# Kernel optimization log

Measured on AMD Instinct MI355X. Metric: run time of the kernel, lower is better.

Reference implementation:

```python
import jax, jax.numpy as jnp
import numpy as np
from jax import lax

B, N, C = 4, 4096, 512
HEADS, SR = 8, 4
HW = 64  # spatial size, HW*HW == N
EPS = 1e-5


def setup_inputs() -> dict:
    key = jax.random.key(0)
    ks = jax.random.split(key, 12)
    s = 0.02
    return {
        "x": jax.random.normal(ks[0], (B, N, C), jnp.float32),
        "wq": jax.random.normal(ks[1], (C, C), jnp.float32) * s,
        "bq": jnp.zeros((C,), jnp.float32),
        "wk": jax.random.normal(ks[2], (C, C), jnp.float32) * s,
        "bk": jnp.zeros((C,), jnp.float32),
        "wv": jax.random.normal(ks[3], (C, C), jnp.float32) * s,
        "bv": jnp.zeros((C,), jnp.float32),
        "w_sr": jax.random.normal(ks[4], (SR, SR, C, C), jnp.float32) * s,  # HWIO
        "b_sr": jnp.zeros((C,), jnp.float32),
        "gamma": jnp.ones((C,), jnp.float32),
        "beta": jnp.zeros((C,), jnp.float32),
        "wp": jax.random.normal(ks[5], (C, C), jnp.float32) * s,
        "bp": jnp.zeros((C,), jnp.float32),
    }


def _layernorm(x, gamma, beta):
    mu = jnp.mean(x, axis=-1, keepdims=True)
    var = jnp.mean(jnp.square(x - mu), axis=-1, keepdims=True)
    return (x - mu) * lax.rsqrt(var + EPS) * gamma + beta


def reference(x, wq, bq, wk, bk, wv, bv, w_sr, b_sr, gamma, beta, wp, bp):
    b, n, c = x.shape
    dh = c // HEADS
    scale = dh ** (-0.5)
    # Q at full resolution: [b, heads, n, dh]
    q = (x @ wq + bq).reshape(b, n, HEADS, dh).transpose(0, 2, 1, 3)
    # spatial reduction of K/V: conv stride=kernel=SR (VALID)
    xr = x.reshape(b, HW, HW, c)
    xr = lax.conv_general_dilated(
        xr, w_sr, window_strides=(SR, SR), padding="VALID",
        dimension_numbers=("NHWC", "HWIO", "NHWC")) + b_sr
    xr = xr.reshape(b, -1, c)  # [b, n_kv, c]
    xr = _layernorm(xr, gamma, beta)
    n_kv = xr.shape[1]
    k = (xr @ wk + bk).reshape(b, n_kv, HEADS, dh).transpose(0, 2, 1, 3)
    v = (xr @ wv + bv).reshape(b, n_kv, HEADS, dh).transpose(0, 2, 1, 3)
    attn = jnp.einsum("bhqd,bhkd->bhqk", q, k) * scale
    attn = jax.nn.softmax(attn, axis=-1)
    out = jnp.einsum("bhqk,bhkd->bhqd", attn, v)
    out = out.transpose(0, 2, 1, 3).reshape(b, n, c)
    return out @ wp + bp
```

## Files before the change

### kernel.cpp

```cpp
#include <hip/hip_runtime.h>
#include <hip/hip_bf16.h>


#define EPSV 1e-5f
#define SCALE_Q 0.18033688011112042f

typedef __attribute__((ext_vector_type(8))) short short8v;
typedef __attribute__((ext_vector_type(4))) short short4v;
typedef __attribute__((ext_vector_type(4))) float float4v;

static __device__ __forceinline__ ushort f2bf_bits(float x) {
  __hip_bfloat16 h = __float2bfloat16(x);
  return *(ushort*)&h;
}

static __device__ __forceinline__ float4v mfma16(short8v a, short8v b, float4v c) {
  return __builtin_amdgcn_mfma_f32_16x16x32_bf16(a, b, c, 0, 0, 0);
}

static __device__ __forceinline__ size_t img_idx(int row, int k, int KC) {
  const int rt = row >> 7, kc = k >> 5, f = (row >> 4) & 7, lid = row & 15;
  const int k32 = k & 31, lg = (k32 >> 2) & 3, j = (k32 & 3) + ((k32 >> 4) & 1) * 4;
  return ((size_t)(rt * KC + kc) * 8 + f) * 512 + (lid + 16 * lg) * 8 + j;
}

static __device__ __forceinline__ void wr_chunk(ushort* lds, int base, int4 v) {
  *(int2*)&lds[base]       = make_int2(v.x, v.y);
  *(int2*)&lds[base + 128] = make_int2(v.z, v.w);
}

__global__ __launch_bounds__(256)
void prep(const float* __restrict__ x, const float* __restrict__ wq,
          const float* __restrict__ wk, const float* __restrict__ wv,
          const float* __restrict__ wp, const float* __restrict__ wsr,
          const float* __restrict__ bk, const float* __restrict__ bv,
          ushort* __restrict__ xbf, ushort* __restrict__ ximg,
          ushort* __restrict__ wqimg, ushort* __restrict__ wkvimg,
          ushort* __restrict__ wpimg, ushort* __restrict__ wsrT,
          float* __restrict__ bkv) {
  __shared__ float t[32][33];
  const int bid = blockIdx.x, tid = threadIdx.x;
  if (bid < 4096) {
    const int i = bid * 256 + tid;
    const float4* s4 = (const float4*)x;
    const float4 a = s4[2 * i], b = s4[2 * i + 1];
    short8v v;
    v[0] = (short)f2bf_bits(a.x); v[1] = (short)f2bf_bits(a.y);
    v[2] = (short)f2bf_bits(a.z); v[3] = (short)f2bf_bits(a.w);
    v[4] = (short)f2bf_bits(b.x); v[5] = (short)f2bf_bits(b.y);
    v[6] = (short)f2bf_bits(b.z); v[7] = (short)f2bf_bits(b.w);
    *(short8v*)&xbf[(size_t)i * 8] = v;
    const int row = i >> 6, c = (i & 63) * 8;
    const int rt = row >> 7, f = (row >> 4) & 7, lid = row & 15;
    const int kc = c >> 5, k32 = c & 31, lg0 = (k32 >> 2) & 3, j0 = ((k32 >> 4) & 1) * 4;
    ushort* basep = ximg + ((size_t)(rt * 16 + kc) * 8 + f) * 512 + j0;
    const int4 vi = *(const int4*)&v;
    *(int2*)&basep[(lid + 16 * lg0) * 8] = make_int2(vi.x, vi.y);
    *(int2*)&basep[(lid + 16 * (lg0 + 1)) * 8] = make_int2(vi.z, vi.w);
  } else if (bid < 8192) {
    const int tI = bid - 4096;
    const int kr0 = (tI & 255) * 32, c0 = (tI >> 8) * 32;
    {
      const int r = tid >> 3, c4 = (tid & 7) * 4;
      const float4 v = *(const float4*)&wsr[(size_t)(kr0 + r) * 512 + c0 + c4];
      t[r][c4 + 0] = v.x; t[r][c4 + 1] = v.y; t[r][c4 + 2] = v.z; t[r][c4 + 3] = v.w;
    }
    __syncthreads();
    {
      const int n = tid >> 3, k4 = (tid & 7) * 4;
      short4v o;
#pragma unroll
      for (int i = 0; i < 4; ++i) o[i] = (short)f2bf_bits(t[k4 + i][n]);
      *(short4v*)&wsrT[(size_t)(c0 + n) * 8192 + kr0 + k4] = o;
    }
  } else if (bid < 9216) {
    const int wsel = (bid - 8192) >> 8;
    const int tI = (bid - 8192) & 255;
    const int kr0 = (tI & 15) * 32, c0 = (tI >> 4) * 32;
    const float* src = wsel == 0 ? wq : wsel == 1 ? wk : wsel == 2 ? wv : wp;
    ushort* dst = wsel == 0 ? wqimg : wsel == 3 ? wpimg : wkvimg;
    const int colbase = (wsel == 2) ? 512 : 0;
    {
      const int r = tid >> 3, c4 = (tid & 7) * 4;
      const float4 v = *(const float4*)&src[(size_t)(kr0 + r) * 512 + c0 + c4];
      t[r][c4 + 0] = v.x; t[r][c4 + 1] = v.y; t[r][c4 + 2] = v.z; t[r][c4 + 3] = v.w;
    }
    __syncthreads();
    {
      const int n = tid >> 3, k4 = (tid & 7) * 4;
      const int col = colbase + c0 + n, k = kr0 + k4;
      short4v o;
#pragma unroll
      for (int i = 0; i < 4; ++i) o[i] = (short)f2bf_bits(t[k4 + i][n]);
      *(short4v*)&dst[img_idx(col, k, 16)] = o;
    }
  } else {
    const int i4 = tid * 4;
    const float4 v = (i4 < 512) ? *(const float4*)&bk[i4] : *(const float4*)&bv[i4 - 512];
    *(float4*)&bkv[i4] = v;
  }
}

static __device__ __forceinline__ int4 ld_patch(const ushort* xbf, int b, int oh, int ow, int kg) {
  const int ij = kg >> 9, ci = kg & 511;
  const int n = (oh * 4 + (ij >> 2)) * 64 + ow * 4 + (ij & 3);
  return *(const int4*)(xbf + ((size_t)b * 4096 + n) * 512 + ci);
}

__global__ __launch_bounds__(256)
void conv_bf(const ushort* __restrict__ xbf, const ushort* __restrict__ wsrT,
             float* __restrict__ part) {
  __shared__ ushort lds[8192];
  const int tid = threadIdx.x;
  const int wave = tid >> 6, lane = tid & 63;
  const int wm = wave >> 1, wn = wave & 1;
  const int bm = blockIdx.x * 128, bn = blockIdx.y * 128, z = blockIdx.z;
  const int lid = lane & 15, lg = lane >> 4;
  const int r0 = tid >> 2, c8 = tid & 3;
  const int g0 = 2 * (c8 & 1), h2 = c8 >> 1;
  const int c0 = c8 * 8;
  const int basew = ((r0 >> 4) * 64 + 16 * g0 + (r0 & 15)) * 8 + h2 * 4;
  const int p0 = bm + r0, p1 = p0 + 64;
  const int b0 = p0 >> 8, oh0 = (p0 & 255) >> 4, ow0 = p0 & 15;
  const int b1 = p1 >> 8, oh1 = (p1 & 255) >> 4, ow1 = p1 & 15;
  const ushort* Br0 = wsrT + (size_t)(bn + r0) * 8192;
  const ushort* Br1 = Br0 + (size_t)64 * 8192;
  float4v acc[4][4];
  const float4v zf = {0.f, 0.f, 0.f, 0.f};
#pragma unroll
  for (int mi = 0; mi < 4; ++mi)
#pragma unroll
    for (int ni = 0; ni < 4; ++ni) acc[mi][ni] = zf;
  int kg = z * 512 + c0;
  int4 pa0 = ld_patch(xbf, b0, oh0, ow0, kg);
  int4 pa1 = ld_patch(xbf, b1, oh1, ow1, kg);
  int4 pb0 = *(const int4*)(Br0 + kg);
  int4 pb1 = *(const int4*)(Br1 + kg);
  for (int kb = 0; kb < 16; ++kb) {
    wr_chunk(lds, basew, pa0);
    wr_chunk(lds, basew + 2048, pa1);
    wr_chunk(lds, basew + 4096, pb0);
    wr_chunk(lds, basew + 6144, pb1);
    __syncthreads();
    if (kb < 15) {
      kg += 32;
      pa0 = ld_patch(xbf, b0, oh0, ow0, kg);
      pa1 = ld_patch(xbf, b1, oh1, ow1, kg);
      pb0 = *(const int4*)(Br0 + kg);
      pb1 = *(const int4*)(Br1 + kg);
    }
    short8v af[4], bfr[4];
#pragma unroll
    for (int mi = 0; mi < 4; ++mi)
      af[mi] = *(const short8v*)&lds[((wm * 4 + mi) * 64 + lane) * 8];
#pragma unroll
    for (int ni = 0; ni < 4; ++ni)
      bfr[ni] = *(const short8v*)&lds[4096 + ((wn * 4 + ni) * 64 + lane) * 8];
#pragma unroll
    for (int mi = 0; mi < 4; ++mi)
#pragma unroll
      for (int ni = 0; ni < 4; ++ni) acc[mi][ni] = mfma16(af[mi], bfr[ni], acc[mi][ni]);
    __syncthreads();
  }
#pragma unroll
  for (int mi = 0; mi < 4; ++mi)
#pragma unroll
    for (int ni = 0; ni < 4; ++ni)
#pragma unroll
      for (int reg = 0; reg < 4; ++reg)
        part[(size_t)(z * 1024 + bm + wm * 64 + mi * 16 + 4 * lg + reg) * 512 +
             bn + wn * 64 + ni * 16 + lid] = acc[mi][ni][reg];
}

__global__ __launch_bounds__(256)
void reduce_ln(const float* __restrict__ part, const float* __restrict__ bsr,
               const float* __restrict__ gamma, const float* __restrict__ beta,
               ushort* __restrict__ xlnimg) {
  const int wave = threadIdx.x >> 6;
  const int lane = threadIdx.x & 63;
  const int row = blockIdx.x * 4 + wave;
  const int c = lane * 8;
  float v[8];
  {
    const float4 a = *(const float4*)&bsr[c];
    const float4 b = *(const float4*)&bsr[c + 4];
    v[0] = a.x; v[1] = a.y; v[2] = a.z; v[3] = a.w;
    v[4] = b.x; v[5] = b.y; v[6] = b.z; v[7] = b.w;
  }
#pragma unroll
  for (int z = 0; z < 16; ++z) {
    const float* pr = &part[((size_t)z * 1024 + row) * 512 + c];
    const float4 a = *(const float4*)pr;
    const float4 b = *(const float4*)(pr + 4);
    v[0] += a.x; v[1] += a.y; v[2] += a.z; v[3] += a.w;
    v[4] += b.x; v[5] += b.y; v[6] += b.z; v[7] += b.w;
  }
  float sum = 0.f;
#pragma unroll
  for (int i = 0; i < 8; ++i) sum += v[i];
#pragma unroll
  for (int off = 32; off >= 1; off >>= 1) sum += __shfl_xor(sum, off);
  const float mu = sum * (1.0f / 512.0f);
  float sq = 0.f;
#pragma unroll
  for (int i = 0; i < 8; ++i) { v[i] -= mu; sq += v[i] * v[i]; }
#pragma unroll
  for (int off = 32; off >= 1; off >>= 1) sq += __shfl_xor(sq, off);
  const float rs = rsqrtf(sq * (1.0f / 512.0f) + EPSV);
  const float4 g1 = *(const float4*)&gamma[c];
  const float4 g2 = *(const float4*)&gamma[c + 4];
  const float4 e1 = *(const float4*)&beta[c];
  const float4 e2 = *(const float4*)&beta[c + 4];
  const float g[8] = {g1.x, g1.y, g1.z, g1.w, g2.x, g2.y, g2.z, g2.w};
  const float e[8] = {e1.x, e1.y, e1.z, e1.w, e2.x, e2.y, e2.z, e2.w};
  short8v ov;
#pragma unroll
  for (int i = 0; i < 8; ++i) ov[i] = (short)f2bf_bits(v[i] * rs * g[i] + e[i]);
  const int rt = row >> 7, f = (row >> 4) & 7, lid = row & 15;
  const int kc = c >> 5, k32 = c & 31, lg0 = (k32 >> 2) & 3, j0 = ((k32 >> 4) & 1) * 4;
  ushort* basep = xlnimg + ((size_t)(rt * 16 + kc) * 8 + f) * 512 + j0;
  const int4 vi = *(const int4*)&ov;
  *(int2*)&basep[(lid + 16 * lg0) * 8] = make_int2(vi.x, vi.y);
  *(int2*)&basep[(lid + 16 * (lg0 + 1)) * 8] = make_int2(vi.z, vi.w);
}

template<int MODE>
__global__ __launch_bounds__(256)
void gemm_img(const ushort* __restrict__ Aimg, const ushort* __restrict__ Bimg,
              const float* __restrict__ bias, void* __restrict__ outp, float scale) {
  constexpr int KC = 16;
  const int tid = threadIdx.x;
  const int wave = tid >> 6, lane = tid & 63;
  const int wm = wave >> 1, wn = wave & 1;
  const int rt = blockIdx.x, ct = blockIdx.y;
  const int lid = lane & 15, lg = lane >> 4;
  const ushort* Ab = Aimg + ((size_t)rt * KC * 8 + wm * 4) * 512 + lane * 8;
  const ushort* Bb = Bimg + ((size_t)ct * KC * 8 + wn * 4) * 512 + lane * 8;
  float4v acc[4][4];
  const float4v zf = {0.f, 0.f, 0.f, 0.f};
#pragma unroll
  for (int mi = 0; mi < 4; ++mi)
#pragma unroll
    for (int ni = 0; ni < 4; ++ni) acc[mi][ni] = zf;
#pragma unroll
  for (int kb = 0; kb < KC; ++kb) {
    short8v af[4], bf[4];
#pragma unroll
    for (int mi = 0; mi < 4; ++mi)
      af[mi] = *(const short8v*)(Ab + (size_t)kb * 4096 + mi * 512);
#pragma unroll
    for (int ni = 0; ni < 4; ++ni)
      bf[ni] = *(const short8v*)(Bb + (size_t)kb * 4096 + ni * 512);
#pragma unroll
    for (int mi = 0; mi < 4; ++mi)
#pragma unroll
      for (int ni = 0; ni < 4; ++ni) acc[mi][ni] = mfma16(af[mi], bf[ni], acc[mi][ni]);
  }
  float bvv[4];
#pragma unroll
  for (int ni = 0; ni < 4; ++ni) bvv[ni] = bias[ct * 128 + wn * 64 + ni * 16 + lid];
#pragma unroll
  for (int mi = 0; mi < 4; ++mi)
#pragma unroll
    for (int ni = 0; ni < 4; ++ni) {
      const int col = ct * 128 + wn * 64 + ni * 16 + lid;
#pragma unroll
      for (int reg = 0; reg < 4; ++reg) {
        const int row = rt * 128 + wm * 64 + mi * 16 + 4 * lg + reg;
        const float v = (acc[mi][ni][reg] + bvv[ni]) * scale;
        if (MODE == 0) {
          ((float*)outp)[(size_t)row * 512 + col] = v;
        } else if (MODE == 2) {
          ushort* img = (ushort*)outp;
          const int bb = row >> 8, kv = row & 255;
          if (col < 512) {
            const int hh = col >> 6, d = col & 63;
            img[(size_t)(bb * 8 + hh) * 16384 +
                ((kv >> 4) * 2 + (d >> 5)) * 512 +
                ((kv & 15) + (((d >> 2) & 3) << 4)) * 8 +
                (d & 3) + (((d >> 4) & 1) << 2)] = f2bf_bits(v);
          } else {
            const int c2 = col - 512;
            const int hh = c2 >> 6, d = c2 & 63;
            (img + 524288)[(size_t)(bb * 8 + hh) * 16384 +
                ((d >> 4) * 8 + (kv >> 5)) * 512 +
                ((d & 15) + (((kv >> 2) & 3) << 4)) * 8 +
                (kv & 3) + (((kv >> 4) & 1) << 2)] = f2bf_bits(v);
          }
        } else {
          ushort* img = (ushort*)outp;
          const int bq_ = row >> 12, n = row & 4095;
          const int qtt = n >> 7, nn = n & 127;
          const int wv_ = nn >> 5, qf = (nn >> 4) & 1, lidq = nn & 15;
          const int h = col >> 6, d = col & 63, tt = d >> 5, d32 = d & 31;
          const int lgq = (d32 >> 2) & 3, jq = (d32 & 3) + ((d32 >> 4) & 1) * 4;
          img[((size_t)(((bq_ * 8 + h) * 32 + qtt) * 4 + wv_) * 4 + qf * 2 + tt) * 512 +
              (lidq + 16 * lgq) * 8 + jq] = f2bf_bits(v);
        }
      }
    }
}

__global__ __launch_bounds__(256)
void attn_img(const ushort* __restrict__ qimg, const ushort* __restrict__ kvimg,
              ushort* __restrict__ oimg) {
  const int bh = blockIdx.x, qt = blockIdx.y;
  const int b = bh >> 3, h = bh & 7;
  const int tid = threadIdx.x;
  const int wave = tid >> 6, lane = tid & 63;
  const int lid = lane & 15, lg = lane >> 4;
  const ushort* kb_ = kvimg + (size_t)bh * 16384;
  const ushort* vb_ = kvimg + 524288 + (size_t)bh * 16384;
  const ushort* qb_ = qimg + ((size_t)((bh * 32 + qt) * 4 + wave) * 4) * 512 + lane * 8;
  short8v qfr[2][2];
#pragma unroll
  for (int qf = 0; qf < 2; ++qf)
#pragma unroll
    for (int t = 0; t < 2; ++t)
      qfr[qf][t] = *(const short8v*)(qb_ + (qf * 2 + t) * 512);
  float4v s[16][2];
  const float4v zf = {0.f, 0.f, 0.f, 0.f};
#pragma unroll
  for (int kvf = 0; kvf < 16; ++kvf) { s[kvf][0] = zf; s[kvf][1] = zf; }
#pragma unroll
  for (int kvf = 0; kvf < 16; ++kvf)
#pragma unroll
    for (int t = 0; t < 2; ++t) {
      const short8v ka = *(const short8v*)(kb_ + ((kvf * 2 + t) * 64 + lane) * 8);
      s[kvf][0] = mfma16(ka, qfr[0][t], s[kvf][0]);
      s[kvf][1] = mfma16(ka, qfr[1][t], s[kvf][1]);
    }
  float inv[2];
#pragma unroll
  for (int qf = 0; qf < 2; ++qf) {
    float m = -1e30f;
#pragma unroll
    for (int kvf = 0; kvf < 16; ++kvf)
#pragma unroll
      for (int e = 0; e < 4; ++e) m = fmaxf(m, s[kvf][qf][e]);
    m = fmaxf(m, __shfl_xor(m, 16));
    m = fmaxf(m, __shfl_xor(m, 32));
    float sum = 0.f;
#pragma unroll
    for (int kvf = 0; kvf < 16; ++kvf)
#pragma unroll
      for (int e = 0; e < 4; ++e) {
        const float p = __builtin_amdgcn_exp2f(s[kvf][qf][e] - m);
        s[kvf][qf][e] = p;
        sum += p;
      }
    sum += __shfl_xor(sum, 16);
    sum += __shfl_xor(sum, 32);
    inv[qf] = 1.0f / sum;
  }
  float4v o[2][4];
#pragma unroll
  for (int qf = 0; qf < 2; ++qf)
#pragma unroll
    for (int nf = 0; nf < 4; ++nf) o[qf][nf] = zf;
#pragma unroll
  for (int t = 0; t < 8; ++t) {
    short8v vb[4];
#pragma unroll
    for (int nf = 0; nf < 4; ++nf)
      vb[nf] = *(const short8v*)(vb_ + ((nf * 8 + t) * 64 + lane) * 8);
#pragma unroll
    for (int qf = 0; qf < 2; ++qf) {
      short8v pa;
#pragma unroll
      for (int j = 0; j < 4; ++j) {
        pa[j]     = (short)f2bf_bits(s[2 * t][qf][j]);
        pa[4 + j] = (short)f2bf_bits(s[2 * t + 1][qf][j]);
      }
#pragma unroll
      for (int nf = 0; nf < 4; ++nf) o[qf][nf] = mfma16(pa, vb[nf], o[qf][nf]);
    }
  }
  const int rt_o = b * 32 + qt;
#pragma unroll
  for (int qf = 0; qf < 2; ++qf) {
    float sc[4];
#pragma unroll
    for (int reg = 0; reg < 4; ++reg) sc[reg] = __shfl(inv[qf], 4 * lg + reg);
    const int f_o = wave * 2 + qf;
#pragma unroll
    for (int nf = 0; nf < 4; ++nf) {
      const int colc = h * 64 + nf * 16 + lid;
      const int kc = colc >> 5, k32 = colc & 31;
      const int lgk = (k32 >> 2) & 3, jk = (k32 & 3) + ((k32 >> 4) & 1) * 4;
      ushort* basep = oimg + ((size_t)(rt_o * 16 + kc) * 8 + f_o) * 512 + 16 * lgk * 8 + jk;
#pragma unroll
      for (int reg = 0; reg < 4; ++reg)
        basep[(4 * lg + reg) * 8] = f2bf_bits(o[qf][nf][reg] * sc[reg]);
    }
  }
}

extern "C" void kernel_launch(void* const* d_in, const int* in_sizes, int n_in,
                              void* d_out, int out_size, void* d_ws, size_t ws_size,
                              hipStream_t stream) {
  const float* x     = (const float*)d_in[0];
  const float* wq    = (const float*)d_in[1];
  const float* bq    = (const float*)d_in[2];
  const float* wk    = (const float*)d_in[3];
  const float* bk    = (const float*)d_in[4];
  const float* wv    = (const float*)d_in[5];
  const float* bv    = (const float*)d_in[6];
  const float* wsr   = (const float*)d_in[7];
  const float* bsr   = (const float*)d_in[8];
  const float* gamma = (const float*)d_in[9];
  const float* beta  = (const float*)d_in[10];
  const float* wp    = (const float*)d_in[11];
  const float* bp    = (const float*)d_in[12];
  float* out = (float*)d_out;

  char* w = (char*)d_ws;
  ushort* xbf    = (ushort*)(w);
  ushort* ximg   = (ushort*)(w + 16777216);
  float*  part   = (float*) (w + 33554432);
  ushort* qimg   = (ushort*)(w + 33554432);
  ushort* oimg   = (ushort*)(w + 50331648);
  ushort* wsrT   = (ushort*)(w + 67108864);
  ushort* wqimg  = (ushort*)(w + 75497472);
  ushort* wpimg  = (ushort*)(w + 76021760);
  ushort* wkvimg = (ushort*)(w + 76546048);
  ushort* xlnimg = (ushort*)(w + 77594624);
  ushort* kvimg  = (ushort*)(w + 78643200);
  float*  bkv    = (float*) (w + 80740352);

  prep<<<9217, 256, 0, stream>>>(x, wq, wk, wv, wp, wsr, bk, bv,
                                 xbf, ximg, wqimg, wkvimg, wpimg, wsrT, bkv);
  conv_bf<<<dim3(8, 4, 16), 256, 0, stream>>>(xbf, wsrT, part);
  reduce_ln<<<256, 256, 0, stream>>>(part, bsr, gamma, beta, xlnimg);
  gemm_img<2><<<dim3(8, 8), 256, 0, stream>>>(xlnimg, wkvimg, bkv, kvimg, 1.0f);
  gemm_img<3><<<dim3(128, 4), 256, 0, stream>>>(ximg, wqimg, bq, qimg, SCALE_Q);
  attn_img<<<dim3(32, 32), 256, 0, stream>>>(qimg, kvimg, oimg);
  gemm_img<0><<<dim3(128, 4), 256, 0, stream>>>(oimg, wpimg, bp, out, 1.0f);
}
```

Baseline: 231.8 us.

## Fuse conv and Q projection into one launch; stage GEMM tiles via global_load_lds

The spatial-reduction conv and the Q projection GEMM now run as one kernel launch of 1024 blocks. The first 512 blocks do the conv partials and the rest compute Q, so two independent GEMMs can fill the GPU together. The conv weight is pre-laid out in the MFMA image format so it can be loaded with direct global-to-LDS loads. The other GEMMs now stage A/B tiles through LDS with global_load_lds instead of reading fragments straight from global memory. Workspace offsets move so that qimg no longer aliases the conv partial buffer. This adds barrier overhead per k-step in exchange for shared reuse and fewer launches.

```diff
diff --git a/kernel.cpp b/kernel.cpp
--- a/kernel.cpp
+++ b/kernel.cpp
@@ -27,6 +27,12 @@
 static __device__ __forceinline__ void wr_chunk(ushort* lds, int base, int4 v) {
   *(int2*)&lds[base]       = make_int2(v.x, v.y);
   *(int2*)&lds[base + 128] = make_int2(v.z, v.w);
+}
+
+static __device__ __forceinline__ void gl_lds16(const ushort* g, ushort* l) {
+  __builtin_amdgcn_global_load_lds(
+      (const __attribute__((address_space(1))) void*)g,
+      (__attribute__((address_space(3))) void*)l, 16, 0, 0);
 }
 
 __global__ __launch_bounds__(256)
@@ -36,7 +42,7 @@
           const float* __restrict__ bk, const float* __restrict__ bv,
           ushort* __restrict__ xbf, ushort* __restrict__ ximg,
           ushort* __restrict__ wqimg, ushort* __restrict__ wkvimg,
-          ushort* __restrict__ wpimg, ushort* __restrict__ wsrT,
+          ushort* __restrict__ wpimg, ushort* __restrict__ wsrimg,
           float* __restrict__ bkv) {
   __shared__ float t[32][33];
   const int bid = blockIdx.x, tid = threadIdx.x;
@@ -71,7 +77,7 @@
       short4v o;
 #pragma unroll
       for (int i = 0; i < 4; ++i) o[i] = (short)f2bf_bits(t[k4 + i][n]);
-      *(short4v*)&wsrT[(size_t)(c0 + n) * 8192 + kr0 + k4] = o;
+      *(short4v*)&wsrimg[img_idx(c0 + n, kr0 + k4, 256)] = o;
     }
   } else if (bid < 9216) {
     const int wsel = (bid - 8192) >> 8;
@@ -88,11 +94,10 @@
     __syncthreads();
     {
       const int n = tid >> 3, k4 = (tid & 7) * 4;
-      const int col = colbase + c0 + n, k = kr0 + k4;
       short4v o;
 #pragma unroll
       for (int i = 0; i < 4; ++i) o[i] = (short)f2bf_bits(t[k4 + i][n]);
-      *(short4v*)&dst[img_idx(col, k, 16)] = o;
+      *(short4v*)&dst[img_idx(colbase + c0 + n, kr0 + k4, 16)] = o;
     }
   } else {
     const int i4 = tid * 4;
@@ -108,68 +113,112 @@
 }
 
 __global__ __launch_bounds__(256)
-void conv_bf(const ushort* __restrict__ xbf, const ushort* __restrict__ wsrT,
-             float* __restrict__ part) {
+void convq(const ushort* __restrict__ xbf, const ushort* __restrict__ wsrimg,
+           float* __restrict__ part, const ushort* __restrict__ ximg,
+           const ushort* __restrict__ wqimg, const float* __restrict__ bq,
+           ushort* __restrict__ qimg) {
   __shared__ ushort lds[8192];
-  const int tid = threadIdx.x;
+  const int bid = blockIdx.x, tid = threadIdx.x;
   const int wave = tid >> 6, lane = tid & 63;
   const int wm = wave >> 1, wn = wave & 1;
-  const int bm = blockIdx.x * 128, bn = blockIdx.y * 128, z = blockIdx.z;
   const int lid = lane & 15, lg = lane >> 4;
-  const int r0 = tid >> 2, c8 = tid & 3;
-  const int g0 = 2 * (c8 & 1), h2 = c8 >> 1;
-  const int c0 = c8 * 8;
-  const int basew = ((r0 >> 4) * 64 + 16 * g0 + (r0 & 15)) * 8 + h2 * 4;
-  const int p0 = bm + r0, p1 = p0 + 64;
-  const int b0 = p0 >> 8, oh0 = (p0 & 255) >> 4, ow0 = p0 & 15;
-  const int b1 = p1 >> 8, oh1 = (p1 & 255) >> 4, ow1 = p1 & 15;
-  const ushort* Br0 = wsrT + (size_t)(bn + r0) * 8192;
-  const ushort* Br1 = Br0 + (size_t)64 * 8192;
+  const int s0 = wave * 2;
   float4v acc[4][4];
   const float4v zf = {0.f, 0.f, 0.f, 0.f};
 #pragma unroll
   for (int mi = 0; mi < 4; ++mi)
 #pragma unroll
     for (int ni = 0; ni < 4; ++ni) acc[mi][ni] = zf;
-  int kg = z * 512 + c0;
-  int4 pa0 = ld_patch(xbf, b0, oh0, ow0, kg);
-  int4 pa1 = ld_patch(xbf, b1, oh1, ow1, kg);
-  int4 pb0 = *(const int4*)(Br0 + kg);
-  int4 pb1 = *(const int4*)(Br1 + kg);
-  for (int kb = 0; kb < 16; ++kb) {
-    wr_chunk(lds, basew, pa0);
-    wr_chunk(lds, basew + 2048, pa1);
-    wr_chunk(lds, basew + 4096, pb0);
-    wr_chunk(lds, basew + 6144, pb1);
-    __syncthreads();
-    if (kb < 15) {
-      kg += 32;
-      pa0 = ld_patch(xbf, b0, oh0, ow0, kg);
-      pa1 = ld_patch(xbf, b1, oh1, ow1, kg);
-      pb0 = *(const int4*)(Br0 + kg);
-      pb1 = *(const int4*)(Br1 + kg);
-    }
-    short8v af[4], bfr[4];
+  if (bid < 512) {
+    const int z = bid >> 5, bm = ((bid >> 2) & 7) * 128, bnn = bid & 3;
+    const int r0 = tid >> 2, c8 = tid & 3, c0 = c8 * 8;
+    const int g0 = 2 * (c8 & 1), h2 = c8 >> 1;
+    const int basew = ((r0 >> 4) * 64 + 16 * g0 + (r0 & 15)) * 8 + h2 * 4;
+    const int p0 = bm + r0, p1 = p0 + 64;
+    const int b0 = p0 >> 8, oh0 = (p0 & 255) >> 4, ow0 = p0 & 15;
+    const int b1 = p1 >> 8, oh1 = (p1 & 255) >> 4, ow1 = p1 & 15;
+    const ushort* Bc = wsrimg + ((size_t)(bnn * 256 + z * 16)) * 4096 + s0 * 512 + lane * 8;
+    int kg = z * 512 + c0;
+    int4 pa0 = ld_patch(xbf, b0, oh0, ow0, kg);
+    int4 pa1 = ld_patch(xbf, b1, oh1, ow1, kg);
+    for (int kb = 0; kb < 16; ++kb) {
+      gl_lds16(Bc + (size_t)kb * 4096,       &lds[4096 + s0 * 512]);
+      gl_lds16(Bc + (size_t)kb * 4096 + 512, &lds[4096 + s0 * 512 + 512]);
+      wr_chunk(lds, basew, pa0);
+      wr_chunk(lds, basew + 2048, pa1);
+      __syncthreads();
+      if (kb < 15) {
+        kg += 32;
+        pa0 = ld_patch(xbf, b0, oh0, ow0, kg);
+        pa1 = ld_patch(xbf, b1, oh1, ow1, kg);
+      }
+      short8v af[4], bf[4];
+#pragma unroll
+      for (int mi = 0; mi < 4; ++mi)
+        af[mi] = *(const short8v*)&lds[((wm * 4 + mi) * 64 + lane) * 8];
+#pragma unroll
+      for (int ni = 0; ni < 4; ++ni)
+        bf[ni] = *(const short8v*)&lds[4096 + ((wn * 4 + ni) * 64 + lane) * 8];
+#pragma unroll
+      for (int mi = 0; mi < 4; ++mi)
+#pragma unroll
+        for (int ni = 0; ni < 4; ++ni) acc[mi][ni] = mfma16(af[mi], bf[ni], acc[mi][ni]);
+      __syncthreads();
+    }
 #pragma unroll
     for (int mi = 0; mi < 4; ++mi)
-      af[mi] = *(const short8v*)&lds[((wm * 4 + mi) * 64 + lane) * 8];
-#pragma unroll
-    for (int ni = 0; ni < 4; ++ni)
-      bfr[ni] = *(const short8v*)&lds[4096 + ((wn * 4 + ni) * 64 + lane) * 8];
+#pragma unroll
+      for (int ni = 0; ni < 4; ++ni)
+#pragma unroll
+        for (int reg = 0; reg < 4; ++reg)
+          part[(size_t)(z * 1024 + bm + wm * 64 + mi * 16 + 4 * lg + reg) * 512 +
+               bnn * 128 + wn * 64 + ni * 16 + lid] = acc[mi][ni][reg];
+  } else {
+    const int qid = bid - 512;
+    const int rt = qid >> 2, ct = qid & 3;
+    const ushort* Ac = ximg + ((size_t)rt * 16) * 4096 + s0 * 512 + lane * 8;
+    const ushort* Bc = wqimg + ((size_t)ct * 16) * 4096 + s0 * 512 + lane * 8;
+    for (int kb = 0; kb < 16; ++kb) {
+      gl_lds16(Ac + (size_t)kb * 4096,       &lds[s0 * 512]);
+      gl_lds16(Ac + (size_t)kb * 4096 + 512, &lds[s0 * 512 + 512]);
+      gl_lds16(Bc + (size_t)kb * 4096,       &lds[4096 + s0 * 512]);
+      gl_lds16(Bc + (size_t)kb * 4096 + 512, &lds[4096 + s0 * 512 + 512]);
+      __syncthreads();
+      short8v af[4], bf[4];
+#pragma unroll
+      for (int mi = 0; mi < 4; ++mi)
+        af[mi] = *(const short8v*)&lds[((wm * 4 + mi) * 64 + lane) * 8];
+#pragma unroll
+      for (int ni = 0; ni < 4; ++ni)
+        bf[ni] = *(const short8v*)&lds[4096 + ((wn * 4 + ni) * 64 + lane) * 8];
+#pragma unroll
+      for (int mi = 0; mi < 4; ++mi)
+#pragma unroll
+        for (int ni = 0; ni < 4; ++ni) acc[mi][ni] = mfma16(af[mi], bf[ni], acc[mi][ni]);
+      __syncthreads();
+    }
+    float bvv[4];
+#pragma unroll
+    for (int ni = 0; ni < 4; ++ni) bvv[ni] = bq[ct * 128 + wn * 64 + ni * 16 + lid];
 #pragma unroll
     for (int mi = 0; mi < 4; ++mi)
 #pragma unroll
-      for (int ni = 0; ni < 4; ++ni) acc[mi][ni] = mfma16(af[mi], bfr[ni], acc[mi][ni]);
-    __syncthreads();
-  }
-#pragma unroll
-  for (int mi = 0; mi < 4; ++mi)
-#pragma unroll
-    for (int ni = 0; ni < 4; ++ni)
-#pragma unroll
-      for (int reg = 0; reg < 4; ++reg)
-        part[(size_t)(z * 1024 + bm + wm * 64 + mi * 16 + 4 * lg + reg) * 512 +
-             bn + wn * 64 + ni * 16 + lid] = acc[mi][ni][reg];
+      for (int ni = 0; ni < 4; ++ni) {
+        const int col = ct * 128 + wn * 64 + ni * 16 + lid;
+#pragma unroll
+        for (int reg = 0; reg < 4; ++reg) {
+          const int row = rt * 128 + wm * 64 + mi * 16 + 4 * lg + reg;
+          const float v = (acc[mi][ni][reg] + bvv[ni]) * SCALE_Q;
+          const int bq_ = row >> 12, n = row & 4095;
+          const int qtt = n >> 7, nn = n & 127;
+          const int wv_ = nn >> 5, qf = (nn >> 4) & 1, lidq = nn & 15;
+          const int h = col >> 6, d = col & 63, tt = d >> 5, d32 = d & 31;
+          const int lgq = (d32 >> 2) & 3, jq = (d32 & 3) + ((d32 >> 4) & 1) * 4;
+          qimg[((size_t)(((bq_ * 8 + h) * 32 + qtt) * 4 + wv_) * 4 + qf * 2 + tt) * 512 +
+               (lidq + 16 * lgq) * 8 + jq] = f2bf_bits(v);
+        }
+      }
+  }
 }
 
 __global__ __launch_bounds__(256)
@@ -226,35 +275,41 @@
 
 template<int MODE>
 __global__ __launch_bounds__(256)
-void gemm_img(const ushort* __restrict__ Aimg, const ushort* __restrict__ Bimg,
+void gemm_lds(const ushort* __restrict__ Aimg, const ushort* __restrict__ Bimg,
               const float* __restrict__ bias, void* __restrict__ outp, float scale) {
-  constexpr int KC = 16;
+  __shared__ ushort lds[8192];
   const int tid = threadIdx.x;
   const int wave = tid >> 6, lane = tid & 63;
   const int wm = wave >> 1, wn = wave & 1;
   const int rt = blockIdx.x, ct = blockIdx.y;
   const int lid = lane & 15, lg = lane >> 4;
-  const ushort* Ab = Aimg + ((size_t)rt * KC * 8 + wm * 4) * 512 + lane * 8;
-  const ushort* Bb = Bimg + ((size_t)ct * KC * 8 + wn * 4) * 512 + lane * 8;
+  const int s0 = wave * 2;
+  const ushort* Ac = Aimg + ((size_t)rt * 16) * 4096 + s0 * 512 + lane * 8;
+  const ushort* Bc = Bimg + ((size_t)ct * 16) * 4096 + s0 * 512 + lane * 8;
   float4v acc[4][4];
   const float4v zf = {0.f, 0.f, 0.f, 0.f};
 #pragma unroll
   for (int mi = 0; mi < 4; ++mi)
 #pragma unroll
     for (int ni = 0; ni < 4; ++ni) acc[mi][ni] = zf;
-#pragma unroll
-  for (int kb = 0; kb < KC; ++kb) {
+  for (int kb = 0; kb < 16; ++kb) {
+    gl_lds16(Ac + (size_t)kb * 4096,       &lds[s0 * 512]);
+    gl_lds16(Ac + (size_t)kb * 4096 + 512, &lds[s0 * 512 + 512]);
+    gl_lds16(Bc + (size_t)kb * 4096,       &lds[4096 + s0 * 512]);
+    gl_lds16(Bc + (size_t)kb * 4096 + 512, &lds[4096 + s0 * 512 + 512]);
+    __syncthreads();
     short8v af[4], bf[4];
 #pragma unroll
     for (int mi = 0; mi < 4; ++mi)
-      af[mi] = *(const short8v*)(Ab + (size_t)kb * 4096 + mi * 512);
+      af[mi] = *(const short8v*)&lds[((wm * 4 + mi) * 64 + lane) * 8];
 #pragma unroll
     for (int ni = 0; ni < 4; ++ni)
-      bf[ni] = *(const short8v*)(Bb + (size_t)kb * 4096 + ni * 512);
+      bf[ni] = *(const short8v*)&lds[4096 + ((wn * 4 + ni) * 64 + lane) * 8];
 #pragma unroll
     for (int mi = 0; mi < 4; ++mi)
 #pragma unroll
       for (int ni = 0; ni < 4; ++ni) acc[mi][ni] = mfma16(af[mi], bf[ni], acc[mi][ni]);
+    __syncthreads();
   }
   float bvv[4];
 #pragma unroll
@@ -270,7 +325,7 @@
         const float v = (acc[mi][ni][reg] + bvv[ni]) * scale;
         if (MODE == 0) {
           ((float*)outp)[(size_t)row * 512 + col] = v;
-        } else if (MODE == 2) {
+        } else {
           ushort* img = (ushort*)outp;
           const int bb = row >> 8, kv = row & 255;
           if (col < 512) {
@@ -287,15 +342,6 @@
                 ((d & 15) + (((kv >> 2) & 3) << 4)) * 8 +
                 (kv & 3) + (((kv >> 4) & 1) << 2)] = f2bf_bits(v);
           }
-        } else {
-          ushort* img = (ushort*)outp;
-          const int bq_ = row >> 12, n = row & 4095;
-          const int qtt = n >> 7, nn = n & 127;
-          const int wv_ = nn >> 5, qf = (nn >> 4) & 1, lidq = nn & 15;
-          const int h = col >> 6, d = col & 63, tt = d >> 5, d32 = d & 31;
-          const int lgq = (d32 >> 2) & 3, jq = (d32 & 3) + ((d32 >> 4) & 1) * 4;
-          img[((size_t)(((bq_ * 8 + h) * 32 + qtt) * 4 + wv_) * 4 + qf * 2 + tt) * 512 +
-              (lidq + 16 * lgq) * 8 + jq] = f2bf_bits(v);
         }
       }
     }
@@ -418,22 +464,21 @@
   ushort* xbf    = (ushort*)(w);
   ushort* ximg   = (ushort*)(w + 16777216);
   float*  part   = (float*) (w + 33554432);
-  ushort* qimg   = (ushort*)(w + 33554432);
-  ushort* oimg   = (ushort*)(w + 50331648);
-  ushort* wsrT   = (ushort*)(w + 67108864);
-  ushort* wqimg  = (ushort*)(w + 75497472);
-  ushort* wpimg  = (ushort*)(w + 76021760);
-  ushort* wkvimg = (ushort*)(w + 76546048);
-  ushort* xlnimg = (ushort*)(w + 77594624);
-  ushort* kvimg  = (ushort*)(w + 78643200);
-  float*  bkv    = (float*) (w + 80740352);
+  ushort* qimg   = (ushort*)(w + 67108864);
+  ushort* oimg   = (ushort*)(w + 83886080);
+  ushort* wsrimg = (ushort*)(w + 100663296);
+  ushort* wqimg  = (ushort*)(w + 109051904);
+  ushort* wpimg  = (ushort*)(w + 109576192);
+  ushort* wkvimg = (ushort*)(w + 110100480);
+  ushort* xlnimg = (ushort*)(w + 111149056);
+  ushort* kvimg  = (ushort*)(w + 112197632);
+  float*  bkv    = (float*) (w + 114294784);
 
   prep<<<9217, 256, 0, stream>>>(x, wq, wk, wv, wp, wsr, bk, bv,
-                                 xbf, ximg, wqimg, wkvimg, wpimg, wsrT, bkv);
-  conv_bf<<<dim3(8, 4, 16), 256, 0, stream>>>(xbf, wsrT, part);
+                                 xbf, ximg, wqimg, wkvimg, wpimg, wsrimg, bkv);
+  convq<<<1024, 256, 0, stream>>>(xbf, wsrimg, part, ximg, wqimg, bq, qimg);
   reduce_ln<<<256, 256, 0, stream>>>(part, bsr, gamma, beta, xlnimg);
-  gemm_img<2><<<dim3(8, 8), 256, 0, stream>>>(xlnimg, wkvimg, bkv, kvimg, 1.0f);
-  gemm_img<3><<<dim3(128, 4), 256, 0, stream>>>(ximg, wqimg, bq, qimg, SCALE_Q);
+  gemm_lds<2><<<dim3(8, 8), 256, 0, stream>>>(xlnimg, wkvimg, bkv, kvimg, 1.0f);
   attn_img<<<dim3(32, 32), 256, 0, stream>>>(qimg, kvimg, oimg);
-  gemm_img<0><<<dim3(128, 4), 256, 0, stream>>>(oimg, wpimg, bp, out, 1.0f);
-}
+  gemm_lds<0><<<dim3(128, 4), 256, 0, stream>>>(oimg, wpimg, bp, out, 1.0f);
+}
```

Measured after the change: 229.3 us. About the same (-1.1%).
